# Optimization experiments

Measured on AMD Instinct MI355X. Metric: run time of the kernel, lower is better.

Reference implementation:

```python
import jax, jax.numpy as jnp
import numpy as np
import math

VOCAB, SEQ, D_MODEL, H, D_FF, N_LAYERS = 32000, 2048, 768, 12, 3072, 6
D_K = D_MODEL // H
EPS = 1e-7


def _pos_encoding(seq, d):
    pos = jnp.arange(seq, dtype=jnp.float32)[:, None]
    i = jnp.arange(d)[None, :]
    rates = 1.0 / jnp.power(10000.0, (2 * (i // 2)).astype(jnp.float32) / d)
    ang = pos * rates
    return jnp.where(i % 2 == 0, jnp.sin(ang), jnp.cos(ang))  # [seq, d]


def _layernorm(x, alpha, beta):
    # faithful to source: scalar alpha/beta, population std, std+eps in denom
    mean = jnp.mean(x, axis=-1, keepdims=True)
    std = jnp.std(x, axis=-1, keepdims=True)
    return alpha * (x - mean) / (std + EPS) + beta


def setup_inputs() -> dict:
    key = jax.random.key(0)
    ks = jax.random.split(key, 16)
    s = 0.02
    d, f, n = D_MODEL, D_FF, N_LAYERS
    inp = {
        'tokens': jax.random.randint(ks[0], (2, SEQ), 0, VOCAB),
        'emb': jax.random.normal(ks[1], (VOCAB, d), jnp.float32) * s,
        'Wq': jax.random.normal(ks[2], (n, d, d), jnp.float32) * s,
        'bq': jnp.zeros((n, d), jnp.float32),
        'Wk': jax.random.normal(ks[3], (n, d, d), jnp.float32) * s,
        'bk': jnp.zeros((n, d), jnp.float32),
        'Wv': jax.random.normal(ks[4], (n, d, d), jnp.float32) * s,
        'bv': jnp.zeros((n, d), jnp.float32),
        'Wo': jax.random.normal(ks[5], (n, d, d), jnp.float32) * s,
        'bo': jnp.zeros((n, d), jnp.float32),
        'W1': jax.random.normal(ks[6], (n, d, f), jnp.float32) * s,
        'b1': jnp.zeros((n, f), jnp.float32),
        'W2': jax.random.normal(ks[7], (n, f, d), jnp.float32) * s,
        'b2': jnp.zeros((n, d), jnp.float32),
        'ln_alpha': jnp.ones((n, 2), jnp.float32),  # source inits alpha AND beta to ones
        'ln_beta': jnp.ones((n, 2), jnp.float32),
    }
    return inp


def reference(tokens, emb, Wq, bq, Wk, bk, Wv, bv, Wo, bo, W1, b1, W2, b2, ln_alpha, ln_beta):
    B, S = tokens.shape
    x = emb[tokens] * math.sqrt(D_MODEL)          # [B,S,D]
    pe = _pos_encoding(SEQ, D_MODEL)[:S]
    x = x + (x + pe)
    for l in range(N_LAYERS):
        # --- self-attention sublayer (pre-norm then residual add) ---
        h = _layernorm(x, ln_alpha[l, 0], ln_beta[l, 0])
        q = (h @ Wq[l] + bq[l]).reshape(B, S, H, D_K)
        k = (h @ Wk[l] + bk[l]).reshape(B, S, H, D_K)
        v = (h @ Wv[l] + bv[l]).reshape(B, S, H, D_K)
        scores = jnp.einsum('bqhd,bkhd->bhqk', q, k) / math.sqrt(D_K)
        attn = jax.nn.softmax(scores, axis=-1)
        o = jnp.einsum('bhqk,bkhd->bqhd', attn, v).reshape(B, S, D_MODEL)
        x = x + (o @ Wo[l] + bo[l])
        # --- feed-forward sublayer ---
        h = _layernorm(x, ln_alpha[l, 1], ln_beta[l, 1])
        ff = jax.nn.relu(h @ W1[l] + b1[l]) @ W2[l] + b2[l]
        x = x + ff
    return x
```

## Files before the change

kernel.cpp:

```cpp
#include <hip/hip_runtime.h>
#include <cstdint>

#define SEQ 2048
#define DM 768
#define NH 12
#define DKH 64
#define DFF 3072
#define NL 6
#define NTOK 4096
#define SM_SCALE 0.18033688f

typedef __attribute__((ext_vector_type(8))) short bf16x8;
typedef __attribute__((ext_vector_type(4))) float f32x4;

static __device__ __forceinline__ unsigned short f2b(float f) {
    unsigned int u = __builtin_bit_cast(unsigned int, f);
    unsigned int lsb = (u >> 16) & 1;
    u += 0x7fffu + lsb;
    return (unsigned short)(u >> 16);
}

static __device__ __forceinline__ unsigned int cvtpk2(float a, float b) {
    unsigned int r;
    asm("v_cvt_pk_bf16_f32 %0, %1, %2" : "=v"(r) : "v"(a), "v"(b));
    return r;
}

__global__ __launch_bounds__(256) void embed_k(const int* __restrict__ tokens,
                                               const float* __restrict__ emb,
                                               float* __restrict__ x)
{
    int srow = blockIdx.y;
    int d = blockIdx.x * 256 + threadIdx.x;
    int s = srow & (SEQ - 1);
    int tok = tokens[srow];
    float val = 2.0f * 27.712812921102035f * emb[(size_t)tok * DM + d];
    int half2 = (d >> 1) * 2;
    float freq = expf(-(float)half2 * (9.210340371976184f / (float)DM));
    float ang = (float)s * freq;
    val += (d & 1) ? cosf(ang) : sinf(ang);
    x[(size_t)srow * DM + d] = val;
}

__global__ __launch_bounds__(256) void ln_k(const float* __restrict__ x,
                                            unsigned short* __restrict__ h,
                                            const float* __restrict__ alpha_p,
                                            const float* __restrict__ beta_p)
{
    int lane = threadIdx.x & 63;
    int wv = threadIdx.x >> 6;
    int row = blockIdx.x * 4 + wv;
    const float* xr = x + (size_t)row * DM;
    float4 v0 = *(const float4*)&xr[lane * 4];
    float4 v1 = *(const float4*)&xr[256 + lane * 4];
    float4 v2 = *(const float4*)&xr[512 + lane * 4];
    float s  = v0.x + v0.y + v0.z + v0.w + v1.x + v1.y + v1.z + v1.w
             + v2.x + v2.y + v2.z + v2.w;
    float sq = v0.x*v0.x + v0.y*v0.y + v0.z*v0.z + v0.w*v0.w
             + v1.x*v1.x + v1.y*v1.y + v1.z*v1.z + v1.w*v1.w
             + v2.x*v2.x + v2.y*v2.y + v2.z*v2.z + v2.w*v2.w;
#pragma unroll
    for (int m = 1; m < 64; m <<= 1) {
        s  += __shfl_xor(s, m);
        sq += __shfl_xor(sq, m);
    }
    float mean = s * (1.0f / DM);
    float var  = sq * (1.0f / DM) - mean * mean;
    float stdv = sqrtf(fmaxf(var, 0.0f));
    float scale = (*alpha_p) / (stdv + 1e-7f);
    float beta  = *beta_p;
    unsigned short* hr = h + (size_t)row * DM;
    ushort4 o;
    o.x = f2b((v0.x - mean) * scale + beta); o.y = f2b((v0.y - mean) * scale + beta);
    o.z = f2b((v0.z - mean) * scale + beta); o.w = f2b((v0.w - mean) * scale + beta);
    *(ushort4*)&hr[lane * 4] = o;
    o.x = f2b((v1.x - mean) * scale + beta); o.y = f2b((v1.y - mean) * scale + beta);
    o.z = f2b((v1.z - mean) * scale + beta); o.w = f2b((v1.w - mean) * scale + beta);
    *(ushort4*)&hr[256 + lane * 4] = o;
    o.x = f2b((v2.x - mean) * scale + beta); o.y = f2b((v2.y - mean) * scale + beta);
    o.z = f2b((v2.z - mean) * scale + beta); o.w = f2b((v2.w - mean) * scale + beta);
    *(ushort4*)&hr[512 + lane * 4] = o;
}

struct WCAll { const float* src[6]; unsigned short* dst[6]; };
__global__ __launch_bounds__(256) void wconv_all_k(WCAll p)
{
    int t = blockIdx.x;
    const float* W; unsigned short* Wt; int K, N, bn, bk;
    if (t < 2304) {
        int mat = t / 576, rem = t % 576;
        W = p.src[mat]; Wt = p.dst[mat]; K = 768; N = 768;
        bn = (rem % 24) * 32; bk = (rem / 24) * 32;
    } else if (t < 4608) {
        int rem = t - 2304;
        W = p.src[4]; Wt = p.dst[4]; K = 768; N = 3072;
        bn = (rem % 96) * 32; bk = (rem / 96) * 32;
    } else {
        int rem = t - 4608;
        W = p.src[5]; Wt = p.dst[5]; K = 3072; N = 768;
        bn = (rem % 24) * 32; bk = (rem / 24) * 32;
    }
    __shared__ float tt[32][33];
    int tx = threadIdx.x & 31, ty = threadIdx.x >> 5;
#pragma unroll
    for (int i = 0; i < 4; ++i)
        tt[ty * 4 + i][tx] = W[(size_t)(bk + ty * 4 + i) * N + bn + tx];
    __syncthreads();
    int n_l = threadIdx.x >> 3;
    int k_l = (threadIdx.x & 7) * 4;
    ushort4 o;
    o.x = f2b(tt[k_l + 0][n_l]); o.y = f2b(tt[k_l + 1][n_l]);
    o.z = f2b(tt[k_l + 2][n_l]); o.w = f2b(tt[k_l + 3][n_l]);
    *(ushort4*)&Wt[(size_t)(bn + n_l) * K + bk + k_l] = o;
}

template<int OUT_MODE>
__device__ __forceinline__ void gemm_mfma_body(
    const unsigned short* __restrict__ A,
    const unsigned short* __restrict__ Bt,
    const float* __restrict__ bias,
    void* __restrict__ Cv,
    int N, int K, int kbeg, int kend, int bm, int bn)
{
    __shared__ unsigned short As[128][64];
    __shared__ unsigned short Bs[128][64];
    const int tid = threadIdx.x;
    const int lane = tid & 63;
    const int w = tid >> 6;
    const int wm = (w >> 1) << 6;
    const int wn = (w & 1) << 6;
    const int rgrp = lane >> 3;
    const int chunk = (lane & 7) ^ rgrp;
    const size_t a_src = (size_t)(bm + w * 32 + rgrp) * K + chunk * 8;
    const size_t b_src = (size_t)(bn + w * 32 + rgrp) * K + chunk * 8;

    f32x4 acc[4][4] = {};

    for (int kt = kbeg; kt < kend; kt += 64) {
        __syncthreads();
#pragma unroll
        for (int i = 0; i < 4; ++i) {
            __builtin_amdgcn_global_load_lds(
                (const __attribute__((address_space(1))) void*)(A + a_src + (size_t)(i * 8) * K + kt),
                (__attribute__((address_space(3))) void*)&As[w * 32 + i * 8][0], 16, 0, 0);
            __builtin_amdgcn_global_load_lds(
                (const __attribute__((address_space(1))) void*)(Bt + b_src + (size_t)(i * 8) * K + kt),
                (__attribute__((address_space(3))) void*)&Bs[w * 32 + i * 8][0], 16, 0, 0);
        }
        __syncthreads();
#pragma unroll
        for (int kk = 0; kk < 2; ++kk) {
            bf16x8 af[4], bfr[4];
            const int kb = kk * 64 + ((lane >> 4) << 4);
#pragma unroll
            for (int i = 0; i < 4; ++i) {
                int m = wm + i * 16 + (lane & 15);
                af[i] = *(const bf16x8*)((const char*)&As[0][0] + m * 128 + (kb ^ ((m & 7) << 4)));
                int n = wn + i * 16 + (lane & 15);
                bfr[i] = *(const bf16x8*)((const char*)&Bs[0][0] + n * 128 + (kb ^ ((n & 7) << 4)));
            }
            __builtin_amdgcn_s_setprio(1);
#pragma unroll
            for (int i = 0; i < 4; ++i)
#pragma unroll
                for (int j = 0; j < 4; ++j)
                    acc[i][j] = __builtin_amdgcn_mfma_f32_16x16x32_bf16(af[i], bfr[j], acc[i][j], 0, 0, 0);
            __builtin_amdgcn_s_setprio(0);
        }
    }
    const int cl = lane & 15, rg = lane >> 4;
#pragma unroll
    for (int i = 0; i < 4; ++i) {
        int row0 = bm + wm + i * 16 + rg * 4;
#pragma unroll
        for (int j = 0; j < 4; ++j) {
            int col = bn + wn + j * 16 + cl;
            float bv = (OUT_MODE == 5 && kbeg > 0) ? 0.0f : bias[col];
            if (OUT_MODE == 4) {
                int bb = row0 >> 11;
                int s  = row0 & 2047;
                int hh = col >> 6, d = col & 63;
                ushort4 o;
                o.x = f2b(acc[i][j][0] + bv); o.y = f2b(acc[i][j][1] + bv);
                o.z = f2b(acc[i][j][2] + bv); o.w = f2b(acc[i][j][3] + bv);
                *(ushort4*)&((unsigned short*)Cv)[(((size_t)(bb * 12 + hh) * 64 + d) << 11) + s] = o;
            } else {
#pragma unroll
                for (int r = 0; r < 4; ++r) {
                    float val = acc[i][j][r] + bv;
                    size_t idx = (size_t)(row0 + r) * N + col;
                    if (OUT_MODE == 2) {
                        ((unsigned short*)Cv)[idx] = f2b(fmaxf(val, 0.0f));
                    } else if (OUT_MODE == 3) {
                        ((unsigned short*)Cv)[idx] = f2b(val);
                    } else if (OUT_MODE == 6) {
                        ((unsigned short*)Cv)[idx] = f2b(val * SM_SCALE);
                    } else if (OUT_MODE == 5) {
                        atomicAdd(&((float*)Cv)[idx], val);
                    } else {
                        ((float*)Cv)[idx] += val;
                    }
                }
            }
        }
    }
}

static __device__ __forceinline__ void xcd_swz_st(int gx, int stag, int& bm, int& bn)
{
    int flat = blockIdx.y * gx + blockIdx.x;
    int nwg = gx * gridDim.y;
    flat += stag;
    if (flat >= nwg) flat -= nwg;
    int wg = (flat & 7) * (nwg >> 3) + (flat >> 3);
    bm = (wg / gx) * 128;
    bn = (wg % gx) * 128;
}

template<int OUT_MODE>
__global__ __launch_bounds__(256) void gemm_b(const unsigned short* __restrict__ A,
                                              const unsigned short* __restrict__ Bt,
                                              const float* __restrict__ bias,
                                              void* __restrict__ C, int N, int K)
{
    int bm, bn; xcd_swz_st(gridDim.x, 0, bm, bn);
    gemm_mfma_body<OUT_MODE>(A, Bt, bias, C, N, K, 0, K, bm, bn);
}

__global__ __launch_bounds__(256) void gemm_sk(const unsigned short* __restrict__ A,
                                               const unsigned short* __restrict__ Bt,
                                               const float* __restrict__ bias,
                                               float* __restrict__ C, int N, int K)
{
    int nwg = gridDim.x * gridDim.y;
    int bm, bn; xcd_swz_st(gridDim.x, blockIdx.z * (nwg >> 1), bm, bn);
    int half = K >> 1;
    gemm_mfma_body<5>(A, Bt, bias, C, N, K, blockIdx.z * half, blockIdx.z * half + half,
                      bm, bn);
}

struct QKVArgsB {
    const unsigned short *wq, *wk, *wv;
    const float *bq, *bk, *bv;
    unsigned short *q, *k, *vt;
};
__global__ __launch_bounds__(256) void gemm_qkv_b(const unsigned short* __restrict__ h, QKVArgsB p)
{
    int bm, bn; xcd_swz_st(gridDim.x, 0, bm, bn);
    if (blockIdx.z == 0)
        gemm_mfma_body<6>(h, p.wq, p.bq, p.q, DM, DM, 0, DM, bm, bn);
    else if (blockIdx.z == 1)
        gemm_mfma_body<3>(h, p.wk, p.bk, p.k, DM, DM, 0, DM, bm, bn);
    else
        gemm_mfma_body<4>(h, p.wv, p.bv, p.vt, DM, DM, 0, DM, bm, bn);
}

__global__ __launch_bounds__(256) void attn_m(const unsigned short* __restrict__ qg,
                                              const unsigned short* __restrict__ kg,
                                              const unsigned short* __restrict__ vt,
                                              unsigned short* __restrict__ og)
{
    __shared__ unsigned short Ks[2][64 * 64];
    __shared__ unsigned short Vs[2][64 * 64];
    __shared__ unsigned short Ps[4 * 16 * 64];
    const int tid = threadIdx.x;
    const int lane = tid & 63;
    const int w = tid >> 6;
    const int cl = lane & 15, g = lane >> 4;
    const int flat = blockIdx.x;
    const int r8 = flat >> 3;
    const int qt = r8 & 31;
    const int hb = ((r8 >> 5) << 3) + (flat & 7);
    const int b = hb >= 12;
    const int h = hb - b * 12;
    const int qrow0 = (b << 11) + qt * 64;
    const int krow0 = (b << 11);
    const int srow8 = lane >> 3;
    const int c8 = (lane & 7) ^ srow8;
    const int swz = (cl & 7) << 4;

    bf16x8 qf[2];
#pragma unroll
    for (int sl = 0; sl < 2; ++sl)
        qf[sl] = *(const bf16x8*)(qg + (size_t)(qrow0 + w * 16 + cl) * DM
                                  + h * 64 + sl * 32 + g * 8);

    bf16x8 ones;
#pragma unroll
    for (int j = 0; j < 8; ++j) ones[j] = (short)0x3F80;

    f32x4 oa[4] = {};
    f32x4 la = {};

    int off[2][4];
#pragma unroll
    for (int sl = 0; sl < 2; ++sl)
#pragma unroll
        for (int ni = 0; ni < 4; ++ni) {
            int row = ni * 16 + cl;
            off[sl][ni] = row * 128 + ((sl * 64 + g * 16) ^ ((row & 7) << 4));
        }
    int paoff[2], pwoff[4];
#pragma unroll
    for (int ks = 0; ks < 2; ++ks)
        paoff[ks] = w * 2048 + cl * 128 + ((ks * 64 + g * 16) ^ swz);
#pragma unroll
    for (int ni = 0; ni < 4; ++ni)
        pwoff[ni] = w * 2048 + cl * 128 + ((ni * 32 + g * 8) ^ swz);
    unsigned short* klds0 = &Ks[0][(w * 16) * 64];
    unsigned short* klds1 = &Ks[1][(w * 16) * 64];
    unsigned short* vlds0 = &Vs[0][(w * 16) * 64];
    unsigned short* vlds1 = &Vs[1][(w * 16) * 64];
    const unsigned short* kp = kg + (size_t)(krow0 + w * 16 + srow8) * DM + h * 64 + c8 * 8;
    const unsigned short* vp = vt + ((size_t)((b * 12 + h) * 64) + w * 16 + srow8) * SEQ + c8 * 8;

#define STAGE(kdst_, vdst_)                                                                    \
    {                                                                                          \
        _Pragma("unroll")                                                                      \
        for (int t = 0; t < 2; ++t) {                                                          \
            __builtin_amdgcn_global_load_lds(                                                  \
                (const __attribute__((address_space(1))) void*)(kp + (size_t)(t * 8) * DM),    \
                (__attribute__((address_space(3))) void*)(kdst_ + t * 8 * 64), 16, 0, 0);      \
            __builtin_amdgcn_global_load_lds(                                                  \
                (const __attribute__((address_space(1))) void*)(vp + (size_t)(t * 8) * SEQ),   \
                (__attribute__((address_space(3))) void*)(vdst_ + t * 8 * 64), 16, 0, 0);      \
        }                                                                                      \
        kp += 64 * DM; vp += 64;                                                               \
    }

    STAGE(klds0, vlds0);
    __syncthreads();

    for (int kt = 0; kt < SEQ / 64; ++kt) {
        const int c = kt & 1;
        const int cb = c << 13;
        if (kt + 1 < SEQ / 64) {
            if (c) STAGE(klds0, vlds0) else STAGE(klds1, vlds1);
        }
        const char* Kc = (const char*)Ks + cb;
        const char* Vc = (const char*)Vs + cb;

        f32x4 st[4] = {};
#pragma unroll
        for (int sl = 0; sl < 2; ++sl) {
            bf16x8 kf[4];
#pragma unroll
            for (int ni = 0; ni < 4; ++ni)
                kf[ni] = *(const bf16x8*)(Kc + off[sl][ni]);
            __builtin_amdgcn_s_setprio(1);
#pragma unroll
            for (int ni = 0; ni < 4; ++ni)
                st[ni] = __builtin_amdgcn_mfma_f32_16x16x32_bf16(kf[ni], qf[sl], st[ni], 0, 0, 0);
            __builtin_amdgcn_s_setprio(0);
        }

#pragma unroll
        for (int ni = 0; ni < 4; ++ni) {
            float p0 = exp2f(st[ni][0]);
            float p1 = exp2f(st[ni][1]);
            float p2 = exp2f(st[ni][2]);
            float p3 = exp2f(st[ni][3]);
            uint2 o2;
            o2.x = cvtpk2(p0, p1);
            o2.y = cvtpk2(p2, p3);
            *(uint2*)((char*)Ps + pwoff[ni]) = o2;
        }
        asm volatile("" ::: "memory");

#pragma unroll
        for (int ks = 0; ks < 2; ++ks) {
            bf16x8 pa, vb[4];
            pa = *(const bf16x8*)((const char*)Ps + paoff[ks]);
#pragma unroll
            for (int nj = 0; nj < 4; ++nj)
                vb[nj] = *(const bf16x8*)(Vc + off[ks][nj]);
            __builtin_amdgcn_s_setprio(1);
#pragma unroll
            for (int nj = 0; nj < 4; ++nj)
                oa[nj] = __builtin_amdgcn_mfma_f32_16x16x32_bf16(pa, vb[nj], oa[nj], 0, 0, 0);
            la = __builtin_amdgcn_mfma_f32_16x16x32_bf16(pa, ones, la, 0, 0, 0);
            __builtin_amdgcn_s_setprio(0);
        }

        __syncthreads();
    }
#undef STAGE

#pragma unroll
    for (int r = 0; r < 4; ++r) {
        float linv = 1.0f / la[r];
        int row = qrow0 + w * 16 + g * 4 + r;
#pragma unroll
        for (int nj = 0; nj < 4; ++nj)
            og[(size_t)row * DM + h * 64 + nj * 16 + cl] = f2b(oa[nj][r] * linv);
    }
}

extern "C" void kernel_launch(void* const* d_in, const int* in_sizes, int n_in,
                              void* d_out, int out_size, void* d_ws, size_t ws_size,
                              hipStream_t stream)
{
    const int*   tokens = (const int*)d_in[0];
    const float* emb    = (const float*)d_in[1];
    const float* Wq     = (const float*)d_in[2];
    const float* bq     = (const float*)d_in[3];
    const float* Wk     = (const float*)d_in[4];
    const float* bk     = (const float*)d_in[5];
    const float* Wv     = (const float*)d_in[6];
    const float* bv     = (const float*)d_in[7];
    const float* Wo     = (const float*)d_in[8];
    const float* bo     = (const float*)d_in[9];
    const float* W1     = (const float*)d_in[10];
    const float* b1     = (const float*)d_in[11];
    const float* W2     = (const float*)d_in[12];
    const float* b2     = (const float*)d_in[13];
    const float* ln_a   = (const float*)d_in[14];
    const float* ln_b   = (const float*)d_in[15];

    float* x = (float*)d_out;
    unsigned short* wq_b = (unsigned short*)d_ws;
    unsigned short* wk_b = wq_b + 589824;
    unsigned short* wv_b = wk_b + 589824;
    unsigned short* wo_b = wv_b + 589824;
    unsigned short* w1_b = wo_b + 589824;
    unsigned short* w2_b = w1_b + 2359296;
    unsigned short* h_b  = w2_b + 2359296;
    unsigned short* ob_b = h_b + 3145728;
    unsigned short* ff_b = ob_b + 3145728;
    unsigned short* q_bf = ff_b + 12582912;
    unsigned short* k_bf = q_bf + 3145728;
    unsigned short* vt_b = k_bf + 3145728;

    embed_k<<<dim3(DM / 256, NTOK), 256, 0, stream>>>(tokens, emb, x);

    for (int l = 0; l < NL; ++l) {
        const size_t wsq = (size_t)l * DM * DM;
        const size_t wsf = (size_t)l * DM * DFF;

        WCAll wc;
        wc.src[0] = Wq + wsq; wc.src[1] = Wk + wsq; wc.src[2] = Wv + wsq;
        wc.src[3] = Wo + wsq; wc.src[4] = W1 + wsf; wc.src[5] = W2 + wsf;
        wc.dst[0] = wq_b; wc.dst[1] = wk_b; wc.dst[2] = wv_b;
        wc.dst[3] = wo_b; wc.dst[4] = w1_b; wc.dst[5] = w2_b;
        wconv_all_k<<<6912, 256, 0, stream>>>(wc);

        ln_k<<<NTOK / 4, 256, 0, stream>>>(x, h_b, ln_a + l * 2 + 0, ln_b + l * 2 + 0);

        QKVArgsB p { wq_b, wk_b, wv_b, bq + l * DM, bk + l * DM, bv + l * DM,
                     q_bf, k_bf, vt_b };
        gemm_qkv_b<<<dim3(DM / 128, NTOK / 128, 3), 256, 0, stream>>>(h_b, p);

        attn_m<<<768, 256, 0, stream>>>(q_bf, k_bf, vt_b, ob_b);

        gemm_sk<<<dim3(DM / 128, NTOK / 128, 2), 256, 0, stream>>>(
            ob_b, wo_b, bo + l * DM, x, DM, DM);

        ln_k<<<NTOK / 4, 256, 0, stream>>>(x, h_b, ln_a + l * 2 + 1, ln_b + l * 2 + 1);

        gemm_b<2><<<dim3(DFF / 128, NTOK / 128), 256, 0, stream>>>(
            h_b, w1_b, b1 + l * DFF, ff_b, DFF, DM);

        gemm_sk<<<dim3(DM / 128, NTOK / 128, 2), 256, 0, stream>>>(
            ff_b, w2_b, b2 + l * DM, x, DM, DFF);
    }
}
```

Measured before the change: 1.282 ms.

## Split attention KV range in two and double query rows per wave, add merge kernel

The attention kernel now processes 128 query rows per block, two 16-row tiles per wave, so each K/V tile loaded into LDS feeds twice the MFMA work. To keep the grid at 768 blocks, the key sequence is split into two halves handled by separate blocks. Each half writes unnormalized fp32 partial outputs and row sums to workspace, and a new merge kernel adds them, normalizes and converts to bf16. In exchange it adds fp32 partial-buffer traffic, an extra kernel launch and higher register pressure. Because no running max is tracked, the sums of the two halves can be added directly.

New measurement: 1.327 ms. +3.5%, slower.

```diff
diff --git a/kernel.cpp b/kernel.cpp
--- a/kernel.cpp
+++ b/kernel.cpp
@@ -258,39 +258,44 @@
 __global__ __launch_bounds__(256) void attn_m(const unsigned short* __restrict__ qg,
                                               const unsigned short* __restrict__ kg,
                                               const unsigned short* __restrict__ vt,
-                                              unsigned short* __restrict__ og)
+                                              float* __restrict__ opart,
+                                              float* __restrict__ lpart)
 {
     __shared__ unsigned short Ks[2][64 * 64];
     __shared__ unsigned short Vs[2][64 * 64];
-    __shared__ unsigned short Ps[4 * 16 * 64];
+    __shared__ unsigned short Ps[4 * 32 * 64];
     const int tid = threadIdx.x;
     const int lane = tid & 63;
     const int w = tid >> 6;
     const int cl = lane & 15, g = lane >> 4;
     const int flat = blockIdx.x;
-    const int r8 = flat >> 3;
-    const int qt = r8 & 31;
-    const int hb = ((r8 >> 5) << 3) + (flat & 7);
+    const int xcd = flat & 7;
+    const int rest = flat >> 3;
+    const int part = rest & 1;
+    const int qt = (rest >> 1) & 15;
+    const int hb = (rest >> 5) * 8 + xcd;
     const int b = hb >= 12;
     const int h = hb - b * 12;
-    const int qrow0 = (b << 11) + qt * 64;
-    const int krow0 = (b << 11);
+    const int qrow0 = (b << 11) + qt * 128;
+    const int krow0 = (b << 11) + part * 1024;
     const int srow8 = lane >> 3;
     const int c8 = (lane & 7) ^ srow8;
     const int swz = (cl & 7) << 4;
 
-    bf16x8 qf[2];
-#pragma unroll
-    for (int sl = 0; sl < 2; ++sl)
-        qf[sl] = *(const bf16x8*)(qg + (size_t)(qrow0 + w * 16 + cl) * DM
-                                  + h * 64 + sl * 32 + g * 8);
+    bf16x8 qf[2][2];
+#pragma unroll
+    for (int mi = 0; mi < 2; ++mi)
+#pragma unroll
+        for (int sl = 0; sl < 2; ++sl)
+            qf[mi][sl] = *(const bf16x8*)(qg + (size_t)(qrow0 + w * 32 + mi * 16 + cl) * DM
+                                          + h * 64 + sl * 32 + g * 8);
 
     bf16x8 ones;
 #pragma unroll
     for (int j = 0; j < 8; ++j) ones[j] = (short)0x3F80;
 
-    f32x4 oa[4] = {};
-    f32x4 la = {};
+    f32x4 oa[2][4] = {};
+    f32x4 la[2] = {};
 
     int off[2][4];
 #pragma unroll
@@ -300,19 +305,23 @@
             int row = ni * 16 + cl;
             off[sl][ni] = row * 128 + ((sl * 64 + g * 16) ^ ((row & 7) << 4));
         }
-    int paoff[2], pwoff[4];
-#pragma unroll
-    for (int ks = 0; ks < 2; ++ks)
-        paoff[ks] = w * 2048 + cl * 128 + ((ks * 64 + g * 16) ^ swz);
-#pragma unroll
-    for (int ni = 0; ni < 4; ++ni)
-        pwoff[ni] = w * 2048 + cl * 128 + ((ni * 32 + g * 8) ^ swz);
+    int paoff[2][2], pwoff[2][4];
+#pragma unroll
+    for (int mi = 0; mi < 2; ++mi) {
+#pragma unroll
+        for (int ks = 0; ks < 2; ++ks)
+            paoff[mi][ks] = w * 4096 + (mi * 16 + cl) * 128 + ((ks * 64 + g * 16) ^ swz);
+#pragma unroll
+        for (int ni = 0; ni < 4; ++ni)
+            pwoff[mi][ni] = w * 4096 + (mi * 16 + cl) * 128 + ((ni * 32 + g * 8) ^ swz);
+    }
     unsigned short* klds0 = &Ks[0][(w * 16) * 64];
     unsigned short* klds1 = &Ks[1][(w * 16) * 64];
     unsigned short* vlds0 = &Vs[0][(w * 16) * 64];
     unsigned short* vlds1 = &Vs[1][(w * 16) * 64];
     const unsigned short* kp = kg + (size_t)(krow0 + w * 16 + srow8) * DM + h * 64 + c8 * 8;
-    const unsigned short* vp = vt + ((size_t)((b * 12 + h) * 64) + w * 16 + srow8) * SEQ + c8 * 8;
+    const unsigned short* vp = vt + ((size_t)((b * 12 + h) * 64) + w * 16 + srow8) * SEQ
+                               + part * 1024 + c8 * 8;
 
 #define STAGE(kdst_, vdst_)                                                                    \
     {                                                                                          \
@@ -331,16 +340,16 @@
     STAGE(klds0, vlds0);
     __syncthreads();
 
-    for (int kt = 0; kt < SEQ / 64; ++kt) {
+    for (int kt = 0; kt < 16; ++kt) {
         const int c = kt & 1;
         const int cb = c << 13;
-        if (kt + 1 < SEQ / 64) {
+        if (kt + 1 < 16) {
             if (c) STAGE(klds0, vlds0) else STAGE(klds1, vlds1);
         }
         const char* Kc = (const char*)Ks + cb;
         const char* Vc = (const char*)Vs + cb;
 
-        f32x4 st[4] = {};
+        f32x4 st[2][4] = {};
 #pragma unroll
         for (int sl = 0; sl < 2; ++sl) {
             bf16x8 kf[4];
@@ -349,36 +358,46 @@
                 kf[ni] = *(const bf16x8*)(Kc + off[sl][ni]);
             __builtin_amdgcn_s_setprio(1);
 #pragma unroll
-            for (int ni = 0; ni < 4; ++ni)
-                st[ni] = __builtin_amdgcn_mfma_f32_16x16x32_bf16(kf[ni], qf[sl], st[ni], 0, 0, 0);
+            for (int mi = 0; mi < 2; ++mi)
+#pragma unroll
+                for (int ni = 0; ni < 4; ++ni)
+                    st[mi][ni] = __builtin_amdgcn_mfma_f32_16x16x32_bf16(kf[ni], qf[mi][sl], st[mi][ni], 0, 0, 0);
             __builtin_amdgcn_s_setprio(0);
         }
 
 #pragma unroll
+        for (int mi = 0; mi < 2; ++mi)
+#pragma unroll
         for (int ni = 0; ni < 4; ++ni) {
-            float p0 = exp2f(st[ni][0]);
-            float p1 = exp2f(st[ni][1]);
-            float p2 = exp2f(st[ni][2]);
-            float p3 = exp2f(st[ni][3]);
+            float p0 = exp2f(st[mi][ni][0]);
+            float p1 = exp2f(st[mi][ni][1]);
+            float p2 = exp2f(st[mi][ni][2]);
+            float p3 = exp2f(st[mi][ni][3]);
             uint2 o2;
             o2.x = cvtpk2(p0, p1);
             o2.y = cvtpk2(p2, p3);
-            *(uint2*)((char*)Ps + pwoff[ni]) = o2;
+            *(uint2*)((char*)Ps + pwoff[mi][ni]) = o2;
         }
         asm volatile("" ::: "memory");
 
 #pragma unroll
         for (int ks = 0; ks < 2; ++ks) {
-            bf16x8 pa, vb[4];
-            pa = *(const bf16x8*)((const char*)Ps + paoff[ks]);
+            bf16x8 pa[2], vb[4];
+#pragma unroll
+            for (int mi = 0; mi < 2; ++mi)
+                pa[mi] = *(const bf16x8*)((const char*)Ps + paoff[mi][ks]);
 #pragma unroll
             for (int nj = 0; nj < 4; ++nj)
                 vb[nj] = *(const bf16x8*)(Vc + off[ks][nj]);
             __builtin_amdgcn_s_setprio(1);
 #pragma unroll
-            for (int nj = 0; nj < 4; ++nj)
-                oa[nj] = __builtin_amdgcn_mfma_f32_16x16x32_bf16(pa, vb[nj], oa[nj], 0, 0, 0);
-            la = __builtin_amdgcn_mfma_f32_16x16x32_bf16(pa, ones, la, 0, 0, 0);
+            for (int mi = 0; mi < 2; ++mi)
+#pragma unroll
+                for (int nj = 0; nj < 4; ++nj)
+                    oa[mi][nj] = __builtin_amdgcn_mfma_f32_16x16x32_bf16(pa[mi], vb[nj], oa[mi][nj], 0, 0, 0);
+#pragma unroll
+            for (int mi = 0; mi < 2; ++mi)
+                la[mi] = __builtin_amdgcn_mfma_f32_16x16x32_bf16(pa[mi], ones, la[mi], 0, 0, 0);
             __builtin_amdgcn_s_setprio(0);
         }
 
@@ -386,14 +405,44 @@
     }
 #undef STAGE
 
+    float* op = opart + (size_t)part * NTOK * DM;
+#pragma unroll
+    for (int mi = 0; mi < 2; ++mi)
 #pragma unroll
     for (int r = 0; r < 4; ++r) {
-        float linv = 1.0f / la[r];
-        int row = qrow0 + w * 16 + g * 4 + r;
+        int row = qrow0 + w * 32 + mi * 16 + g * 4 + r;
 #pragma unroll
         for (int nj = 0; nj < 4; ++nj)
-            og[(size_t)row * DM + h * 64 + nj * 16 + cl] = f2b(oa[nj][r] * linv);
-    }
+            op[(size_t)row * DM + h * 64 + nj * 16 + cl] = oa[mi][nj][r];
+    }
+    if (cl == 0) {
+#pragma unroll
+        for (int mi = 0; mi < 2; ++mi)
+#pragma unroll
+        for (int r = 0; r < 4; ++r) {
+            int row = qrow0 + w * 32 + mi * 16 + g * 4 + r;
+            lpart[(size_t)part * NTOK * NH + (size_t)row * NH + h] = la[mi][r];
+        }
+    }
+}
+
+__global__ __launch_bounds__(192) void merge_k(const float* __restrict__ opart,
+                                               const float* __restrict__ lpart,
+                                               unsigned short* __restrict__ ob)
+{
+    int row = blockIdx.x;
+    int d = threadIdx.x * 4;
+    int h = d >> 6;
+    float l = lpart[(size_t)row * NH + h] + lpart[(size_t)NTOK * NH + (size_t)row * NH + h];
+    float linv = 1.0f / l;
+    float4 o0 = *(const float4*)&opart[(size_t)row * DM + d];
+    float4 o1 = *(const float4*)&opart[(size_t)NTOK * DM + (size_t)row * DM + d];
+    ushort4 o;
+    o.x = f2b((o0.x + o1.x) * linv);
+    o.y = f2b((o0.y + o1.y) * linv);
+    o.z = f2b((o0.z + o1.z) * linv);
+    o.w = f2b((o0.w + o1.w) * linv);
+    *(ushort4*)&ob[(size_t)row * DM + d] = o;
 }
 
 extern "C" void kernel_launch(void* const* d_in, const int* in_sizes, int n_in,
@@ -430,6 +479,8 @@
     unsigned short* q_bf = ff_b + 12582912;
     unsigned short* k_bf = q_bf + 3145728;
     unsigned short* vt_b = k_bf + 3145728;
+    float* opart = (float*)(vt_b + 3145728);
+    float* lpart = opart + 2 * 3145728;
 
     embed_k<<<dim3(DM / 256, NTOK), 256, 0, stream>>>(tokens, emb, x);
 
@@ -450,7 +501,8 @@
                      q_bf, k_bf, vt_b };
         gemm_qkv_b<<<dim3(DM / 128, NTOK / 128, 3), 256, 0, stream>>>(h_b, p);
 
-        attn_m<<<768, 256, 0, stream>>>(q_bf, k_bf, vt_b, ob_b);
+        attn_m<<<768, 256, 0, stream>>>(q_bf, k_bf, vt_b, opart, lpart);
+        merge_k<<<NTOK, 192, 0, stream>>>(opart, lpart, ob_b);
 
         gemm_sk<<<dim3(DM / 128, NTOK / 128, 2), 256, 0, stream>>>(
             ob_b, wo_b, bo + l * DM, x, DM, DM);
```
